# Performance work log

Hardware: AMD Instinct MI355X
Metric: run time of the kernel (lower is better)

Reference implementation:

```python
import jax, jax.numpy as jnp
import numpy as np

B, S, D_IN, D_OUT = 4, 2048, 4096, 4096


def setup_inputs() -> dict:
    key = jax.random.key(0)
    k1, k2, k3 = jax.random.split(key, 3)
    # int32 activations (already quantized upstream in the original pipeline)
    x_i32 = jax.random.randint(k1, (B, S, D_IN), -128, 128, dtype=jnp.int32)
    # int8 weights in [in, out] layout (Linear weight transposed), symmetric range [-127, 127]
    weight_i8 = jax.random.randint(k2, (D_IN, D_OUT), -127, 128, dtype=jnp.int32).astype(jnp.int8)
    # bias quantized affine to int32 (scale=16 in original)
    bias_i32 = jax.random.randint(k3, (D_OUT,), -2048, 2048, dtype=jnp.int32)
    return {"x_i32": x_i32, "weight_i8": weight_i8, "bias_i32": bias_i32, "out_shift": 7}


def reference(x_i32, weight_i8, bias_i32, out_shift):
    x_shape = x_i32.shape
    x2d = x_i32.reshape(-1, x_shape[-1]).astype(jnp.int32)  # [tokens, d_in]
    # int8 weights upcast to int32, plain int32 matmul with int32 accumulation
    y = jnp.matmul(x2d, weight_i8.astype(jnp.int32), preferred_element_type=jnp.int32)
    y = y + bias_i32  # fused bias add (int32)
    if out_shift > 0:  # out_shift is a static Python int
        y = jnp.right_shift(y, out_shift)  # arithmetic shift on signed int32
    return y.reshape(*x_shape[:-1], y.shape[-1]).astype(jnp.int32)
```

## Files before the change

### kernel.cpp

```cpp
#include <hip/hip_runtime.h>

using int32x4 = __attribute__((ext_vector_type(4))) int;

#define BM 256
#define BN 256
#define MBUF 65536

__global__ __launch_bounds__(256) void pack_x_kernel(const int32x4* __restrict__ x,
                                                     int32x4* __restrict__ xp,
                                                     int nvec) {
    int t = blockIdx.x * 256 + threadIdx.x;
    if (t >= nvec) return;
    int32x4 a = x[t * 4 + 0];
    int32x4 b = x[t * 4 + 1];
    int32x4 c = x[t * 4 + 2];
    int32x4 d = x[t * 4 + 3];
    int32x4 o;
    o.x = (a.x & 255) | ((a.y & 255) << 8) | ((a.z & 255) << 16) | (a.w << 24);
    o.y = (b.x & 255) | ((b.y & 255) << 8) | ((b.z & 255) << 16) | (b.w << 24);
    o.z = (c.x & 255) | ((c.y & 255) << 8) | ((c.z & 255) << 16) | (c.w << 24);
    o.w = (d.x & 255) | ((d.y & 255) << 8) | ((d.z & 255) << 16) | (d.w << 24);
    xp[t] = o;
}

__global__ __launch_bounds__(256) void transform_w_kernel(const int* __restrict__ w,
                                                          unsigned char* __restrict__ wt,
                                                          int K, int N) {
    __shared__ unsigned char tileT[64][72];
    int tx = threadIdx.x & 15;
    int ty = threadIdx.x >> 4;
    int n0 = blockIdx.x * 64;
    int k0 = blockIdx.y * 64;
#pragma unroll
    for (int r = 0; r < 4; ++r) {
        int row = ty * 4 + r;
        int32x4 v = *(const int32x4*)&w[(size_t)(k0 + row) * N + n0 + tx * 4];
        tileT[tx * 4 + 0][row] = (unsigned char)(v.x & 255);
        tileT[tx * 4 + 1][row] = (unsigned char)(v.y & 255);
        tileT[tx * 4 + 2][row] = (unsigned char)(v.z & 255);
        tileT[tx * 4 + 3][row] = (unsigned char)(v.w & 255);
    }
    __syncthreads();
#pragma unroll
    for (int r = 0; r < 4; ++r) {
        int row = ty * 4 + r;
        uchar4 v = *(const uchar4*)&tileT[row][tx * 4];
        *(uchar4*)&wt[(size_t)(n0 + row) * K + k0 + tx * 4] = v;
    }
}

__global__ __launch_bounds__(512, 2) void gemm_i8_mega(
    const char* __restrict__ A,
    const char* __restrict__ Bt,
    const int* __restrict__ bias,
    const int* __restrict__ shiftp,
    int* __restrict__ C,
    int M, int N, int K) {
    __shared__ char smem[2 * MBUF];

    const int nbn = N / BN;
    const int nwg = gridDim.x;
    const int bid = blockIdx.x;
    const int cpx = nwg >> 3;
    const int swz = (bid & 7) * cpx + (bid >> 3);
    const int m0 = (swz / nbn) * BM;
    const int n0 = (swz % nbn) * BN;

    const int t = threadIdx.x;
    const int lane = t & 63;
    const int wave = t >> 6;
    const int wr = wave >> 2;
    const int wc = wave & 3;

    const int s_row = t >> 3;
    const int s_col = (((t & 7) ^ ((t >> 3) & 7)) << 4);
    const char* a_src = A + (size_t)(m0 + s_row) * K + s_col;
    const char* b_src = Bt + (size_t)(n0 + s_row) * K + s_col;
    const size_t jstr = (size_t)64 * K;
    char* lds_st = smem + t * 16;

    const int lr = lane & 15;
    const int lc = (lane >> 4) << 4;
    const int xr = (lr & 7) << 4;
    const int rowA = (wr << 7) + lr;
    const int rowB = (wc << 6) + lr;
    const int a_s0 = rowA * 128 + (lc ^ xr);
    const int a_s1 = rowA * 128 + ((lc | 64) ^ xr);
    const int b_s0 = 32768 + rowB * 128 + (lc ^ xr);
    const int b_s1 = 32768 + rowB * 128 + ((lc | 64) ^ xr);

    int32x4 acc[8][4] = {};
    int32x4 afX[4], afY[4], bfX[4], bfY[4];

    const int nt = K / 128;

#define GLL(src, dst)                                                 \
    __builtin_amdgcn_global_load_lds(                                 \
        (const __attribute__((address_space(1))) void*)(src),        \
        (__attribute__((address_space(3))) void*)(dst), 16, 0, 0)

#define FENCE asm volatile("" ::: "memory")
#define BARR                           \
    do {                               \
        FENCE;                         \
        __builtin_amdgcn_s_barrier();  \
        FENCE;                         \
    } while (0)
#define SB0 __builtin_amdgcn_sched_barrier(0)
#define LGKM(n)                                                   \
    do {                                                          \
        asm volatile("s_waitcnt lgkmcnt(" #n ")" ::: "memory");   \
        SB0;                                                      \
    } while (0)
#define VMW(n)                                                  \
    do {                                                        \
        asm volatile("s_waitcnt vmcnt(" #n ")" ::: "memory");   \
        SB0;                                                    \
    } while (0)

#define STAGE8(TT, BUF)                                                    \
    do {                                                                   \
        const size_t kc_ = (size_t)(TT) * 128;                             \
        _Pragma("unroll") for (int j = 0; j < 4; ++j)                      \
            GLL(a_src + kc_ + j * jstr, lds_st + (BUF) + j * 8192);        \
        _Pragma("unroll") for (int j = 0; j < 4; ++j)                      \
            GLL(b_src + kc_ + j * jstr, lds_st + (BUF) + 32768 + j * 8192);\
    } while (0)

#define MFMA_B(ACCROW, AF, BF)                                                   \
    do {                                                                         \
        __builtin_amdgcn_s_setprio(1);                                           \
        _Pragma("unroll") for (int mi = 0; mi < 4; ++mi)                         \
            _Pragma("unroll") for (int ni = 0; ni < 4; ++ni)                     \
                acc[(ACCROW) + mi][ni] = __builtin_amdgcn_mfma_i32_16x16x64_i8(  \
                    AF[mi], BF[ni], acc[(ACCROW) + mi][ni], 0, 0, 0);            \
        __builtin_amdgcn_s_setprio(0);                                           \
    } while (0)

#define BODY(BUF)                                                                \
    do {                                                                         \
        _Pragma("unroll") for (int i = 0; i < 4; ++i)                            \
            afX[i] = *(const int32x4*)&smem[(BUF) + a_s0 + i * 2048];            \
        _Pragma("unroll") for (int i = 0; i < 4; ++i)                            \
            bfX[i] = *(const int32x4*)&smem[(BUF) + b_s0 + i * 2048];            \
        _Pragma("unroll") for (int i = 0; i < 4; ++i)                            \
            afY[i] = *(const int32x4*)&smem[(BUF) + a_s0 + (4 + i) * 2048];      \
        _Pragma("unroll") for (int i = 0; i < 4; ++i)                            \
            bfY[i] = *(const int32x4*)&smem[(BUF) + b_s1 + i * 2048];            \
        LGKM(8);                           \
        MFMA_B(0, afX, bfX);                                                     \
        LGKM(4);                                                  \
        _Pragma("unroll") for (int i = 0; i < 4; ++i)                            \
            afX[i] = *(const int32x4*)&smem[(BUF) + a_s1 + i * 2048];            \
        MFMA_B(4, afY, bfX);                                                     \
        LGKM(4);                               \
        _Pragma("unroll") for (int i = 0; i < 4; ++i)                            \
            afY[i] = *(const int32x4*)&smem[(BUF) + a_s1 + (4 + i) * 2048];      \
        LGKM(4);                            \
        MFMA_B(0, afX, bfY);                                                     \
        LGKM(0);                                               \
        MFMA_B(4, afY, bfY);                                                     \
    } while (0)

    STAGE8(0, 0);
    STAGE8(1, MBUF);
    VMW(8);
    BARR;

    for (int tt = 0; tt < nt - 2; tt += 2) {
        BODY(0);
        BARR;
        STAGE8(tt + 2, 0);
        VMW(8);
        BARR;
        BODY(MBUF);
        BARR;
        STAGE8(tt + 3, MBUF);
        VMW(8);
        BARR;
    }
    BODY(0);
    BARR;
    VMW(0);
    BARR;
    BODY(MBUF);

    const int s = *shiftp;
    const int crow = (lane >> 4) << 2;
    const int ccol = lane & 15;
    int bv[4];
#pragma unroll
    for (int nf = 0; nf < 4; ++nf) bv[nf] = bias[n0 + wc * 64 + nf * 16 + ccol];
#pragma unroll
    for (int mf = 0; mf < 8; ++mf) {
        const int grow0 = m0 + wr * 128 + mf * 16 + crow;
#pragma unroll
        for (int nf = 0; nf < 4; ++nf) {
            const int gcol = n0 + wc * 64 + nf * 16 + ccol;
#pragma unroll
            for (int r = 0; r < 4; ++r) {
                int y = acc[mf][nf][r] + bv[nf];
                y = (s > 0) ? (y >> s) : y;
                C[(size_t)(grow0 + r) * N + gcol] = y;
            }
        }
    }
#undef GLL
#undef FENCE
#undef BARR
#undef SB0
#undef LGKM
#undef VMW
#undef STAGE8
#undef MFMA_B
#undef BODY
}

extern "C" void kernel_launch(void* const* d_in, const int* in_sizes, int n_in,
                              void* d_out, int out_size, void* d_ws, size_t ws_size,
                              hipStream_t stream) {
    const int* x = (const int*)d_in[0];
    const int* w = (const int*)d_in[1];
    const int* bias = (const int*)d_in[2];
    const int* shiftp = (const int*)d_in[3];
    int* out = (int*)d_out;

    const int N = in_sizes[2];
    const int K = in_sizes[1] / N;
    const int M = in_sizes[0] / K;

    char* xp = (char*)d_ws;
    unsigned char* wt = (unsigned char*)d_ws + (size_t)M * K;

    int nvec = (int)(((long long)M * K) / 16);
    pack_x_kernel<<<(nvec + 255) / 256, 256, 0, stream>>>((const int32x4*)x, (int32x4*)xp, nvec);

    dim3 tgrid(N / 64, K / 64);
    transform_w_kernel<<<tgrid, 256, 0, stream>>>(w, wt, K, N);

    int nwg = (M / BM) * (N / BN);
    gemm_i8_mega<<<nwg, 512, 0, stream>>>(xp, (const char*)wt, bias, shiftp, out, M, N, K);
}
```

Measured before the change: 184.9 us.

## Shrink GEMM tile to 256x128 with triple-buffered LDS ping-pong pipeline

Halves the N tile to 128, so the 512-thread workgroup now covers 256x128 with 8 waves in a 4x2 layout, each owning a 64x64 sub-tile. Double buffering is replaced by a three-buffer rotation. Global-to-LDS loads for tile t+2 are split into chunks interleaved between the MFMA phases, with barriers around each phase to overlap memory and compute. This doubles the workgroup count and cuts accumulator registers, but lowers arithmetic intensity per tile and adds more barriers.

```diff
diff --git a/kernel.cpp b/kernel.cpp
--- a/kernel.cpp
+++ b/kernel.cpp
@@ -3,8 +3,8 @@
 using int32x4 = __attribute__((ext_vector_type(4))) int;
 
 #define BM 256
-#define BN 256
-#define MBUF 65536
+#define BN 128
+#define BUFSZ 49152
 
 __global__ __launch_bounds__(256) void pack_x_kernel(const int32x4* __restrict__ x,
                                                      int32x4* __restrict__ xp,
@@ -49,14 +49,14 @@
     }
 }
 
-__global__ __launch_bounds__(512, 2) void gemm_i8_mega(
+__global__ __launch_bounds__(512, 2) void gemm_i8_4p(
     const char* __restrict__ A,
     const char* __restrict__ Bt,
     const int* __restrict__ bias,
     const int* __restrict__ shiftp,
     int* __restrict__ C,
     int M, int N, int K) {
-    __shared__ char smem[2 * MBUF];
+    __shared__ char smem[3 * BUFSZ];
 
     const int nbn = N / BN;
     const int nwg = gridDim.x;
@@ -69,8 +69,8 @@
     const int t = threadIdx.x;
     const int lane = t & 63;
     const int wave = t >> 6;
-    const int wr = wave >> 2;
-    const int wc = wave & 3;
+    const int wr = wave >> 1;
+    const int wc = wave & 1;
 
     const int s_row = t >> 3;
     const int s_col = (((t & 7) ^ ((t >> 3) & 7)) << 4);
@@ -82,15 +82,15 @@
     const int lr = lane & 15;
     const int lc = (lane >> 4) << 4;
     const int xr = (lr & 7) << 4;
-    const int rowA = (wr << 7) + lr;
+    const int rowA = (wr << 6) + lr;
     const int rowB = (wc << 6) + lr;
     const int a_s0 = rowA * 128 + (lc ^ xr);
     const int a_s1 = rowA * 128 + ((lc | 64) ^ xr);
     const int b_s0 = 32768 + rowB * 128 + (lc ^ xr);
     const int b_s1 = 32768 + rowB * 128 + ((lc | 64) ^ xr);
 
-    int32x4 acc[8][4] = {};
-    int32x4 afX[4], afY[4], bfX[4], bfY[4];
+    int32x4 acc[4][4] = {};
+    int32x4 afX[4], afY[4], bfX[2], bfY[2];
 
     const int nt = K / 128;
 
@@ -118,72 +118,92 @@
         SB0;                                                    \
     } while (0)
 
-#define STAGE8(TT, BUF)                                                    \
-    do {                                                                   \
-        const size_t kc_ = (size_t)(TT) * 128;                             \
-        _Pragma("unroll") for (int j = 0; j < 4; ++j)                      \
-            GLL(a_src + kc_ + j * jstr, lds_st + (BUF) + j * 8192);        \
-        _Pragma("unroll") for (int j = 0; j < 4; ++j)                      \
-            GLL(b_src + kc_ + j * jstr, lds_st + (BUF) + 32768 + j * 8192);\
-    } while (0)
-
-#define MFMA_B(ACCROW, AF, BF)                                                   \
+#define MFMA8(AF, BF, NC)                                                        \
     do {                                                                         \
         __builtin_amdgcn_s_setprio(1);                                           \
         _Pragma("unroll") for (int mi = 0; mi < 4; ++mi)                         \
-            _Pragma("unroll") for (int ni = 0; ni < 4; ++ni)                     \
-                acc[(ACCROW) + mi][ni] = __builtin_amdgcn_mfma_i32_16x16x64_i8(  \
-                    AF[mi], BF[ni], acc[(ACCROW) + mi][ni], 0, 0, 0);            \
+            _Pragma("unroll") for (int nj = 0; nj < 2; ++nj)                     \
+                acc[mi][(NC) + nj] = __builtin_amdgcn_mfma_i32_16x16x64_i8(      \
+                    AF[mi], BF[nj], acc[mi][(NC) + nj], 0, 0, 0);                \
         __builtin_amdgcn_s_setprio(0);                                           \
     } while (0)
 
-#define BODY(BUF)                                                                \
-    do {                                                                         \
-        _Pragma("unroll") for (int i = 0; i < 4; ++i)                            \
-            afX[i] = *(const int32x4*)&smem[(BUF) + a_s0 + i * 2048];            \
-        _Pragma("unroll") for (int i = 0; i < 4; ++i)                            \
-            bfX[i] = *(const int32x4*)&smem[(BUF) + b_s0 + i * 2048];            \
-        _Pragma("unroll") for (int i = 0; i < 4; ++i)                            \
-            afY[i] = *(const int32x4*)&smem[(BUF) + a_s0 + (4 + i) * 2048];      \
-        _Pragma("unroll") for (int i = 0; i < 4; ++i)                            \
-            bfY[i] = *(const int32x4*)&smem[(BUF) + b_s1 + i * 2048];            \
-        LGKM(8);                           \
-        MFMA_B(0, afX, bfX);                                                     \
-        LGKM(4);                                                  \
-        _Pragma("unroll") for (int i = 0; i < 4; ++i)                            \
-            afX[i] = *(const int32x4*)&smem[(BUF) + a_s1 + i * 2048];            \
-        MFMA_B(4, afY, bfX);                                                     \
-        LGKM(4);                               \
-        _Pragma("unroll") for (int i = 0; i < 4; ++i)                            \
-            afY[i] = *(const int32x4*)&smem[(BUF) + a_s1 + (4 + i) * 2048];      \
-        LGKM(4);                            \
-        MFMA_B(0, afX, bfY);                                                     \
-        LGKM(0);                                               \
-        MFMA_B(4, afY, bfY);                                                     \
-    } while (0)
-
-    STAGE8(0, 0);
-    STAGE8(1, MBUF);
-    VMW(8);
+#define STAGE6(TT, BUF)                                                       \
+    do {                                                                      \
+        const size_t kc_ = (size_t)(TT) * 128;                                \
+        _Pragma("unroll") for (int j = 0; j < 4; ++j)                         \
+            GLL(a_src + kc_ + j * jstr, lds_st + (BUF) + j * 8192);           \
+        _Pragma("unroll") for (int j = 0; j < 2; ++j)                         \
+            GLL(b_src + kc_ + j * jstr, lds_st + (BUF) + 32768 + j * 8192);   \
+    } while (0)
+
+#define TILE(BA, BB, BC, TT, ST, WTAIL, RN)                                        \
+    do {                                                                           \
+        const size_t kc_ = (size_t)((TT) + 2) * 128;                               \
+                                 \
+        _Pragma("unroll") for (int i = 0; i < 2; ++i)                              \
+            bfY[i] = *(const int32x4*)&smem[(BA) + b_s0 + (2 + i) * 2048];         \
+        if (ST) {                                                                  \
+            GLL(a_src + kc_, lds_st + (BC));                                       \
+            GLL(a_src + kc_ + jstr, lds_st + (BC) + 8192);                         \
+        }                                                                          \
+        BARR; LGKM(2);                                                             \
+        MFMA8(afX, bfX, 0);                                        \
+        BARR;                                                                      \
+                      \
+        _Pragma("unroll") for (int i = 0; i < 4; ++i)                              \
+            afY[i] = *(const int32x4*)&smem[(BA) + a_s1 + i * 2048];               \
+        _Pragma("unroll") for (int i = 0; i < 2; ++i)                              \
+            bfX[i] = *(const int32x4*)&smem[(BA) + b_s1 + i * 2048];               \
+        if (ST) {                                                                  \
+            GLL(a_src + kc_ + 2 * jstr, lds_st + (BC) + 16384);                    \
+            GLL(a_src + kc_ + 3 * jstr, lds_st + (BC) + 24576);                    \
+        }                                                                          \
+        BARR; LGKM(6);                                                             \
+        MFMA8(afX, bfY, 2);                                        \
+        BARR;                                                                      \
+                            \
+        _Pragma("unroll") for (int i = 0; i < 2; ++i)                              \
+            bfY[i] = *(const int32x4*)&smem[(BA) + b_s1 + (2 + i) * 2048];         \
+        if (ST) {                                                                  \
+            GLL(b_src + kc_, lds_st + (BC) + 32768);                               \
+            GLL(b_src + kc_ + jstr, lds_st + (BC) + 40960);                        \
+        }                                                                          \
+        BARR; LGKM(2);                                                             \
+        MFMA8(afY, bfX, 0);                                        \
+        WTAIL;          \
+        BARR;                                                                      \
+                               \
+        if (RN) {                                                                  \
+            _Pragma("unroll") for (int i = 0; i < 4; ++i)                          \
+                afX[i] = *(const int32x4*)&smem[(BB) + a_s0 + i * 2048];           \
+            _Pragma("unroll") for (int i = 0; i < 2; ++i)                          \
+                bfX[i] = *(const int32x4*)&smem[(BB) + b_s0 + i * 2048];           \
+        }                                                                          \
+        BARR;                                                                      \
+        if (RN) { LGKM(6); } else { LGKM(0); }                                     \
+        MFMA8(afY, bfY, 2);                                        \
+        BARR;                                                                      \
+    } while (0)
+
+    STAGE6(0, 0);
+    STAGE6(1, BUFSZ);
+    VMW(6);
     BARR;
-
-    for (int tt = 0; tt < nt - 2; tt += 2) {
-        BODY(0);
-        BARR;
-        STAGE8(tt + 2, 0);
-        VMW(8);
-        BARR;
-        BODY(MBUF);
-        BARR;
-        STAGE8(tt + 3, MBUF);
-        VMW(8);
-        BARR;
-    }
-    BODY(0);
-    BARR;
-    VMW(0);
-    BARR;
-    BODY(MBUF);
+#pragma unroll
+    for (int i = 0; i < 4; ++i) afX[i] = *(const int32x4*)&smem[a_s0 + i * 2048];
+#pragma unroll
+    for (int i = 0; i < 2; ++i) bfX[i] = *(const int32x4*)&smem[b_s0 + i * 2048];
+    LGKM(0);
+
+    int ba = 0, bb = BUFSZ, bc = 2 * BUFSZ;
+    for (int tt = 0; tt < nt - 2; ++tt) {
+        TILE(ba, bb, bc, tt, 1, VMW(6), 1);
+        int tmp = ba; ba = bb; bb = bc; bc = tmp;
+    }
+    TILE(ba, bb, bc, nt - 2, 0, VMW(0), 1);
+    { int tmp = ba; ba = bb; bb = bc; bc = tmp; }
+    TILE(ba, bb, bc, nt - 1, 0, (void)0, 0);
 
     const int s = *shiftp;
     const int crow = (lane >> 4) << 2;
@@ -192,8 +212,8 @@
 #pragma unroll
     for (int nf = 0; nf < 4; ++nf) bv[nf] = bias[n0 + wc * 64 + nf * 16 + ccol];
 #pragma unroll
-    for (int mf = 0; mf < 8; ++mf) {
-        const int grow0 = m0 + wr * 128 + mf * 16 + crow;
+    for (int mf = 0; mf < 4; ++mf) {
+        const int grow0 = m0 + wr * 64 + mf * 16 + crow;
 #pragma unroll
         for (int nf = 0; nf < 4; ++nf) {
             const int gcol = n0 + wc * 64 + nf * 16 + ccol;
@@ -211,9 +231,9 @@
 #undef SB0
 #undef LGKM
 #undef VMW
-#undef STAGE8
-#undef MFMA_B
-#undef BODY
+#undef MFMA8
+#undef STAGE6
+#undef TILE
 }
 
 extern "C" void kernel_launch(void* const* d_in, const int* in_sizes, int n_in,
@@ -239,5 +259,5 @@
     transform_w_kernel<<<tgrid, 256, 0, stream>>>(w, wt, K, N);
 
     int nwg = (M / BM) * (N / BN);
-    gemm_i8_mega<<<nwg, 512, 0, stream>>>(xp, (const char*)wt, bias, shiftp, out, M, N, K);
-}
+    gemm_i8_4p<<<nwg, 512, 0, stream>>>(xp, (const char*)wt, bias, shiftp, out, M, N, K);
+}
```

Result: slower. 199.6 us (+7.9%).
